# Kernel optimization log

Measured on AMD Instinct MI355X. Metric: run time of the kernel, lower is better.

Reference implementation:

```python
import jax, jax.numpy as jnp
import numpy as np

N_NODES = 50000
N_EDGES = 800000
IN_FEAT = 256
OUT_FEAT = 256
NUM_RELS = 64
NUM_BASES = 8


def setup_inputs() -> dict:
    key = jax.random.key(0)
    ks = jax.random.split(key, 9)
    x = jax.random.normal(ks[0], (N_NODES, IN_FEAT), dtype=jnp.float32)
    src = jax.random.randint(ks[1], (N_EDGES,), 0, N_NODES, dtype=jnp.int32)
    dst = jax.random.randint(ks[2], (N_EDGES,), 0, N_NODES, dtype=jnp.int32)
    etypes = jax.random.randint(ks[3], (N_EDGES,), 0, NUM_RELS, dtype=jnp.int32)
    norm = jax.random.uniform(ks[4], (N_EDGES, 1), dtype=jnp.float32)
    # glorot-style params
    s_w = (6.0 / (IN_FEAT + OUT_FEAT)) ** 0.5
    weight = jax.random.uniform(ks[5], (NUM_BASES, IN_FEAT, OUT_FEAT), jnp.float32, -s_w, s_w)
    s_c = (6.0 / (NUM_RELS + NUM_BASES)) ** 0.5
    w_comp = jax.random.uniform(ks[6], (NUM_RELS, NUM_BASES), jnp.float32, -s_c, s_c)
    h_bias = jnp.zeros((OUT_FEAT,), jnp.float32)
    loop_weight = jax.random.uniform(ks[7], (IN_FEAT, OUT_FEAT), jnp.float32, -s_w, s_w)
    return {"x": x, "src": src, "dst": dst, "etypes": etypes, "norm": norm,
            "weight": weight, "w_comp": w_comp, "h_bias": h_bias,
            "loop_weight": loop_weight}


def reference(x, src, dst, etypes, norm, weight, w_comp, h_bias, loop_weight):
    # Basis regularizer with num_bases < num_rels:
    #   W_r = sum_b w_comp[r, b] * V_b
    # Per-edge message: msg_e = (x[src_e] @ W_{etype_e}) * norm_e,
    # aggregated by sum onto destination nodes. Since the map is linear,
    # we aggregate per basis first, then apply V_b (8 dense GEMMs).
    n_nodes = x.shape[0]
    coef = w_comp[etypes]                      # [E, B] per-edge basis coeffs
    xs = x[src] * norm                         # [E, D] normalized source feats
    out = jnp.zeros((n_nodes, weight.shape[2]), x.dtype)
    for b in range(weight.shape[0]):           # small fixed loop over bases
        agg = jax.ops.segment_sum(xs * coef[:, b:b + 1], dst,
                                  num_segments=n_nodes)   # [N, D]
        out = out + agg @ weight[b]            # [N, O]
    out = out + h_bias + x @ loop_weight       # bias + self-loop
    return jax.nn.relu(out)
```

## Files before the change

kernel.cpp:

```cpp
#include <hip/hip_runtime.h>
#include <hip/hip_bf16.h>
#include <stdint.h>

#define N_NODES 50000
#define N_EDGES 800000
#define IN_FEAT 256
#define OUT_FEAT 256
#define NUM_RELS 64
#define NUM_BASES 8
#define KTOT 2304
#define KAGG 2048
#define MP 50048
#define SCAN_BLKS 196

typedef __attribute__((ext_vector_type(8))) __bf16 bf16x8;
typedef __attribute__((ext_vector_type(4))) __bf16 bf16x4;
typedef __attribute__((ext_vector_type(4))) float f32x4;
typedef __attribute__((ext_vector_type(2))) float f32x2;

static __device__ __forceinline__ void gload_lds16(const void* g, void* l) {
  auto gp = (const __attribute__((address_space(1))) void*)(uintptr_t)g;
  auto lp = (__attribute__((address_space(3))) void*)(uint32_t)(uintptr_t)l;
  __builtin_amdgcn_global_load_lds(gp, lp, 16, 0, 0);
}

__global__ void k_prex(const float* __restrict__ x, __bf16* __restrict__ xb) {
  int i = blockIdx.x * 256 + threadIdx.x;
  const float4* xp = (const float4*)x;
  float4 u = xp[i * 2], v = xp[i * 2 + 1];
  bf16x8 o;
  o[0] = (__bf16)u.x; o[1] = (__bf16)u.y; o[2] = (__bf16)u.z; o[3] = (__bf16)u.w;
  o[4] = (__bf16)v.x; o[5] = (__bf16)v.y; o[6] = (__bf16)v.z; o[7] = (__bf16)v.w;
  *(bf16x8*)(xb + (size_t)i * 8) = o;
}

__global__ void k_count(const int* __restrict__ dst, int* __restrict__ deg) {
  int e = blockIdx.x * 256 + threadIdx.x;
  atomicAdd(&deg[dst[e]], 1);
}

__global__ void k_scan1(const int* __restrict__ deg, int* __restrict__ offs,
                        int* __restrict__ bsum) {
  __shared__ int s[256];
  int t = threadIdx.x;
  int i = blockIdx.x * 256 + t;
  int v = (i < N_NODES) ? deg[i] : 0;
  s[t] = v;
  __syncthreads();
  for (int d = 1; d < 256; d <<= 1) {
    int y = (t >= d) ? s[t - d] : 0;
    __syncthreads();
    s[t] += y;
    __syncthreads();
  }
  if (i < N_NODES) offs[i] = s[t] - v;
  if (t == 255) bsum[blockIdx.x] = s[255];
}

__global__ void k_scan3(int* __restrict__ offs, const int* __restrict__ bsum,
                        int* __restrict__ fill) {
  __shared__ int s[256];
  int t = threadIdx.x;
  s[t] = (t < SCAN_BLKS && t < blockIdx.x) ? bsum[t] : 0;
  __syncthreads();
  for (int d = 128; d; d >>= 1) {
    if (t < d) s[t] += s[t + d];
    __syncthreads();
  }
  int base = s[0];
  int i = blockIdx.x * 256 + t;
  if (i < N_NODES) {
    int o = offs[i] + base;
    offs[i] = o;
    fill[i] = o;
  }
}

__global__ void k_scatter(const int* __restrict__ dst, const int* __restrict__ srcv,
                          const int* __restrict__ ety, const float* __restrict__ norm,
                          int* __restrict__ fill, uint2* __restrict__ erec) {
  int e = blockIdx.x * 256 + threadIdx.x;
  int pos = atomicAdd(&fill[dst[e]], 1);
  erec[pos] = make_uint2((unsigned)srcv[e] | ((unsigned)ety[e] << 16),
                         __float_as_uint(norm[e]));
}

#define AGG_BODY(RX, RY, XV)                                                  \
  do {                                                                        \
    int et_ = (RX) >> 16;                                                     \
    float nm_ = __uint_as_float(RY);                                          \
    f32x2 v0_ = {__uint_as_float((XV).x << 16) * nm_,                         \
                 __uint_as_float((XV).x & 0xffff0000u) * nm_};                 \
    f32x2 v1_ = {__uint_as_float((XV).y << 16) * nm_,                         \
                 __uint_as_float((XV).y & 0xffff0000u) * nm_};                 \
    f32x4 cl_ = *(const f32x4*)&wc[et_ * 8];                                  \
    f32x4 ch_ = *(const f32x4*)&wc[et_ * 8 + 4];                              \
    _Pragma("unroll") for (int b = 0; b < 4; ++b) {                           \
      acc[b][0] += v0_ * cl_[b];                                              \
      acc[b][1] += v1_ * cl_[b];                                              \
      acc[b + 4][0] += v0_ * ch_[b];                                          \
      acc[b + 4][1] += v1_ * ch_[b];                                          \
    }                                                                         \
  } while (0)

__global__ __launch_bounds__(256) void k_agg(
    const __bf16* __restrict__ xb, const float* __restrict__ w_comp,
    const int* __restrict__ offs, const int* __restrict__ fin,
    const uint2* __restrict__ erec, __bf16* __restrict__ A) {
  __shared__ float wc[NUM_RELS * NUM_BASES];
  int t = threadIdx.x;
  wc[t] = w_comp[t];
  wc[t + 256] = w_comp[t + 256];
  __syncthreads();

  int wid = t >> 6, lane = t & 63;
  int node = blockIdx.x * 4 + wid;

  f32x2 acc[NUM_BASES][2];
#pragma unroll
  for (int b = 0; b < NUM_BASES; ++b) {
    acc[b][0] = f32x2{0.f, 0.f};
    acc[b][1] = f32x2{0.f, 0.f};
  }

  int i0 = offs[node];
  int cnt = fin[node] - i0;
  const uint2* rp = erec + i0;
  int lo4 = lane * 4;

  int i = 0;
  for (; i + 8 <= cnt; i += 8) {
    uint2 r[8];
#pragma unroll
    for (int j = 0; j < 8; ++j) r[j] = rp[i + j];
    uint2 xv[8];
#pragma unroll
    for (int j = 0; j < 8; ++j)
      xv[j] = *(const uint2*)(xb + (size_t)(r[j].x & 0xffff) * IN_FEAT + lo4);
#pragma unroll
    for (int j = 0; j < 8; ++j) AGG_BODY(r[j].x, r[j].y, xv[j]);
  }
  for (; i + 4 <= cnt; i += 4) {
    uint2 r[4];
#pragma unroll
    for (int j = 0; j < 4; ++j) r[j] = rp[i + j];
    uint2 xv[4];
#pragma unroll
    for (int j = 0; j < 4; ++j)
      xv[j] = *(const uint2*)(xb + (size_t)(r[j].x & 0xffff) * IN_FEAT + lo4);
#pragma unroll
    for (int j = 0; j < 4; ++j) AGG_BODY(r[j].x, r[j].y, xv[j]);
  }
  for (; i < cnt; ++i) {
    uint2 r = rp[i];
    uint2 xv = *(const uint2*)(xb + (size_t)(r.x & 0xffff) * IN_FEAT + lo4);
    AGG_BODY(r.x, r.y, xv);
  }

  __bf16* Ar = A + (size_t)node * KAGG + lo4;
#pragma unroll
  for (int b = 0; b < NUM_BASES; ++b) {
    bf16x4 o;
    o[0] = (__bf16)acc[b][0][0];
    o[1] = (__bf16)acc[b][0][1];
    o[2] = (__bf16)acc[b][1][0];
    o[3] = (__bf16)acc[b][1][1];
    *(bf16x4*)(Ar + b * 256) = o;
  }
}

__global__ void k_prepw(const float* __restrict__ weight, const float* __restrict__ loop_w,
                        __bf16* __restrict__ Wt) {
  int o = blockIdx.x;
  int t = threadIdx.x;
#pragma unroll
  for (int c = 0; c < 9; ++c) {
    int r = c * 256 + t;
    float v = (r < 2048) ? weight[(size_t)r * 256 + o]
                         : loop_w[(size_t)(r - 2048) * 256 + o];
    Wt[(size_t)o * KTOT + r] = (__bf16)v;
  }
}

__global__ __launch_bounds__(256, 1) void k_gemm(const __bf16* __restrict__ A,
                                                 const __bf16* __restrict__ xb,
                                                 const __bf16* __restrict__ Wt,
                                                 const float* __restrict__ bias,
                                                 float* __restrict__ out) {
  __shared__ __align__(16) __bf16 sA[3 * 128 * 64];
  __shared__ __align__(16) __bf16 sB[3 * 256 * 64];

  int t = threadIdx.x;
  int wid = t >> 6, lane = t & 63;
  int tm = blockIdx.x;
  int wr = wid >> 1, wc = wid & 1;
  int rfw = __builtin_amdgcn_readfirstlane(wid);

  f32x4 acc[4][8];
#pragma unroll
  for (int m = 0; m < 4; ++m)
#pragma unroll
    for (int n = 0; n < 8; ++n) acc[m][n] = f32x4{0.f, 0.f, 0.f, 0.f};

  int frow = lane & 15;
  int g = lane >> 4;
  int f7 = lane & 7;
  int kb0 = ((g ^ f7) << 4);
  int kb1 = (((4 + g) ^ f7) << 4);

  int qoff = ((t & 7) ^ ((t >> 3) & 7)) * 8;
  const __bf16* gaP[4];
  const __bf16* gxP[4];
#pragma unroll
  for (int it = 0; it < 4; ++it) {
    int row = it * 32 + (t >> 3);
    gaP[it] = A + (size_t)(tm * 128 + row) * KAGG + qoff;
    gxP[it] = xb + (size_t)(tm * 128 + row) * IN_FEAT + qoff;
  }
  const __bf16* gbP[8];
#pragma unroll
  for (int it = 0; it < 8; ++it) {
    int row = it * 32 + (t >> 3);
    gbP[it] = Wt + (size_t)row * KTOT + qoff;
  }

#define VMWAIT(N) asm volatile("s_waitcnt vmcnt(" #N ")" ::: "memory")
#define BARRIER()                                   \
  do {                                              \
    asm volatile("" ::: "memory");                  \
    __builtin_amdgcn_s_barrier();                   \
    asm volatile("" ::: "memory");                  \
  } while (0)

#define STAGE(KT, BUF)                                                        \
  do {                                                                        \
    int k0_ = (KT) * 64;                                                      \
    char* bA_ = (char*)sA + (BUF) * 16384;                                    \
    char* bB_ = (char*)sB + (BUF) * 32768;                                    \
    if ((KT) < 32) {                                                          \
      _Pragma("unroll") for (int it = 0; it < 4; ++it)                        \
          gload_lds16(gaP[it] + k0_, bA_ + (it * 256 + rfw * 64) * 16);       \
    } else {                                                                  \
      int kx_ = k0_ - KAGG;                                                   \
      _Pragma("unroll") for (int it = 0; it < 4; ++it)                        \
          gload_lds16(gxP[it] + kx_, bA_ + (it * 256 + rfw * 64) * 16);       \
    }                                                                         \
    _Pragma("unroll") for (int it = 0; it < 8; ++it)                          \
        gload_lds16(gbP[it] + k0_, bB_ + (it * 256 + rfw * 64) * 16);         \
  } while (0)

#define COMPUTE(BUF)                                                          \
  do {                                                                        \
    const char* bA_ = (const char*)sA + (BUF) * 16384;                        \
    const char* bB_ = (const char*)sB + (BUF) * 32768;                        \
    {                                                                         \
      bf16x8 af[4], bfr[8];                                                   \
      _Pragma("unroll") for (int m = 0; m < 4; ++m)                           \
          af[m] = *(const bf16x8*)(bA_ + (wr * 64 + m * 16 + frow) * 128 + kb0);\
      _Pragma("unroll") for (int n = 0; n < 8; ++n)                           \
          bfr[n] = *(const bf16x8*)(bB_ + (wc * 128 + n * 16 + frow) * 128 + kb0);\
      _Pragma("unroll") for (int m = 0; m < 4; ++m)                           \
          _Pragma("unroll") for (int n = 0; n < 8; ++n)                       \
              acc[m][n] = __builtin_amdgcn_mfma_f32_16x16x32_bf16(            \
                  af[m], bfr[n], acc[m][n], 0, 0, 0);                         \
    }                                                                         \
    {                                                                         \
      bf16x8 af[4], bfr[8];                                                   \
      _Pragma("unroll") for (int m = 0; m < 4; ++m)                           \
          af[m] = *(const bf16x8*)(bA_ + (wr * 64 + m * 16 + frow) * 128 + kb1);\
      _Pragma("unroll") for (int n = 0; n < 8; ++n)                           \
          bfr[n] = *(const bf16x8*)(bB_ + (wc * 128 + n * 16 + frow) * 128 + kb1);\
      _Pragma("unroll") for (int m = 0; m < 4; ++m)                           \
          _Pragma("unroll") for (int n = 0; n < 8; ++n)                       \
              acc[m][n] = __builtin_amdgcn_mfma_f32_16x16x32_bf16(            \
                  af[m], bfr[n], acc[m][n], 0, 0, 0);                         \
    }                                                                         \
  } while (0)

  STAGE(0, 0);
  STAGE(1, 1);
  STAGE(2, 2);

#define STEP(KT, BUF)                                                         \
  do {                                                                        \
    VMWAIT(24);          \
    BARRIER();                       \
    COMPUTE(BUF);                                                             \
    BARRIER();               \
    STAGE((KT) + 3, BUF);                                                     \
  } while (0)

  for (int k3 = 0; k3 < 33; k3 += 3) {
    STEP(k3 + 0, 0);
    STEP(k3 + 1, 1);
    STEP(k3 + 2, 2);
  }
  VMWAIT(24); BARRIER(); COMPUTE(0);
  VMWAIT(12); BARRIER(); COMPUTE(1);
  VMWAIT(0);  BARRIER(); COMPUTE(2);
#undef STEP
#undef STAGE
#undef COMPUTE
#undef VMWAIT
#undef BARRIER

  int r0 = (lane >> 4) * 4;
  int c0 = lane & 15;
#pragma unroll
  for (int m = 0; m < 4; ++m) {
    int rowb = tm * 128 + wr * 64 + m * 16 + r0;
#pragma unroll
    for (int n = 0; n < 8; ++n) {
      int col = wc * 128 + n * 16 + c0;
      float bv = bias[col];
#pragma unroll
      for (int r = 0; r < 4; ++r) {
        int row = rowb + r;
        if (row < N_NODES) {
          float v = acc[m][n][r] + bv;
          out[(size_t)row * OUT_FEAT + col] = v > 0.f ? v : 0.f;
        }
      }
    }
  }
}

extern "C" void kernel_launch(void* const* d_in, const int* in_sizes, int n_in,
                              void* d_out, int out_size, void* d_ws, size_t ws_size,
                              hipStream_t stream) {
  const float* x      = (const float*)d_in[0];
  const int*   src    = (const int*)d_in[1];
  const int*   dst    = (const int*)d_in[2];
  const int*   ety    = (const int*)d_in[3];
  const float* norm   = (const float*)d_in[4];
  const float* weight = (const float*)d_in[5];
  const float* w_comp = (const float*)d_in[6];
  const float* h_bias = (const float*)d_in[7];
  const float* loop_w = (const float*)d_in[8];
  float* out = (float*)d_out;

  char* ws = (char*)d_ws;
  __bf16* A  = (__bf16*)ws;
  size_t off = (size_t)MP * KAGG * 2;
  __bf16* xb = (__bf16*)(ws + off);
  off += (size_t)MP * IN_FEAT * 2;
  __bf16* Wt = (__bf16*)(ws + off);
  off += (size_t)256 * KTOT * 2;
  uint2* erec = (uint2*)(ws + off);
  off += (size_t)N_EDGES * 8;
  int* deg   = (int*)(ws + off);
  int* offs  = deg + N_NODES;
  int* fill  = offs + N_NODES;
  int* bsum  = fill + N_NODES;

  hipMemsetAsync(deg, 0, N_NODES * sizeof(int), stream);
  k_prex<<<(N_NODES * IN_FEAT / 8) / 256, 256, 0, stream>>>(x, xb);
  k_count<<<N_EDGES / 256, 256, 0, stream>>>(dst, deg);
  k_scan1<<<SCAN_BLKS, 256, 0, stream>>>(deg, offs, bsum);
  k_scan3<<<SCAN_BLKS, 256, 0, stream>>>(offs, bsum, fill);
  k_scatter<<<N_EDGES / 256, 256, 0, stream>>>(dst, src, ety, norm, fill, erec);
  k_agg<<<N_NODES / 4, 256, 0, stream>>>(xb, w_comp, offs, fill, erec, A);
  k_prepw<<<256, 256, 0, stream>>>(weight, loop_w, Wt);
  k_gemm<<<MP / 128, 256, 0, stream>>>(A, xb, Wt, h_bias, out);
}
```

Baseline: 328.7 us.

## Use 256x256 GEMM tile with 8 waves and interleaved double-buffered schedule

The fused GEMM is reworked to process 256-row tiles with 512 threads, a 2-buffer LDS pipeline, and an interleaved schedule that splits each k-step into four MFMA groups. Global-to-LDS loads for the next tiles are issued between them, and MFMA sections run at raised wave priority. This is meant to improve overlap of loads with matrix math and raise reuse of the weight tile. In exchange it halves the number of blocks, which can leave CUs idle, and the padded row count grows.

```diff
diff --git a/kernel.cpp b/kernel.cpp
--- a/kernel.cpp
+++ b/kernel.cpp
@@ -10,7 +10,8 @@
 #define NUM_BASES 8
 #define KTOT 2304
 #define KAGG 2048
-#define MP 50048
+#define MP 50176
+#define NT 36
 #define SCAN_BLKS 196
 
 typedef __attribute__((ext_vector_type(8))) __bf16 bf16x8;
@@ -182,136 +183,159 @@
   }
 }
 
-__global__ __launch_bounds__(256, 1) void k_gemm(const __bf16* __restrict__ A,
+__global__ __launch_bounds__(512, 1) void k_gemm(const __bf16* __restrict__ A,
                                                  const __bf16* __restrict__ xb,
                                                  const __bf16* __restrict__ Wt,
                                                  const float* __restrict__ bias,
                                                  float* __restrict__ out) {
-  __shared__ __align__(16) __bf16 sA[3 * 128 * 64];
-  __shared__ __align__(16) __bf16 sB[3 * 256 * 64];
+  __shared__ __align__(16) __bf16 sA[2 * 256 * 64];
+  __shared__ __align__(16) __bf16 sB[2 * 256 * 64];
 
   int t = threadIdx.x;
   int wid = t >> 6, lane = t & 63;
   int tm = blockIdx.x;
-  int wr = wid >> 1, wc = wid & 1;
+  int wr = wid >> 2;
+  int wcol = wid & 3;
   int rfw = __builtin_amdgcn_readfirstlane(wid);
 
-  f32x4 acc[4][8];
-#pragma unroll
-  for (int m = 0; m < 4; ++m)
-#pragma unroll
-    for (int n = 0; n < 8; ++n) acc[m][n] = f32x4{0.f, 0.f, 0.f, 0.f};
+  f32x4 acc[8][4];
+#pragma unroll
+  for (int m = 0; m < 8; ++m)
+#pragma unroll
+    for (int n = 0; n < 4; ++n) acc[m][n] = f32x4{0.f, 0.f, 0.f, 0.f};
 
   int frow = lane & 15;
   int g = lane >> 4;
-  int f7 = lane & 7;
+  int f7 = frow & 7;
   int kb0 = ((g ^ f7) << 4);
   int kb1 = (((4 + g) ^ f7) << 4);
 
-  int qoff = ((t & 7) ^ ((t >> 3) & 7)) * 8;
-  const __bf16* gaP[4];
-  const __bf16* gxP[4];
-#pragma unroll
-  for (int it = 0; it < 4; ++it) {
-    int row = it * 32 + (t >> 3);
-    gaP[it] = A + (size_t)(tm * 128 + row) * KAGG + qoff;
-    gxP[it] = xb + (size_t)(tm * 128 + row) * IN_FEAT + qoff;
-  }
-  const __bf16* gbP[8];
-#pragma unroll
-  for (int it = 0; it < 8; ++it) {
-    int row = it * 32 + (t >> 3);
-    gbP[it] = Wt + (size_t)row * KTOT + qoff;
-  }
+  int rh = t >> 3;
+  int qoff = ((t & 7) ^ (rh & 7)) * 8;
+  const __bf16* gA[2][2];
+  const __bf16* gX[2][2];
+  const __bf16* gB[2][2];
+#pragma unroll
+  for (int h = 0; h < 2; ++h)
+#pragma unroll
+    for (int it = 0; it < 2; ++it) {
+      int row = h * 128 + it * 64 + rh;
+      gA[h][it] = A + (size_t)(tm * 256 + row) * KAGG + qoff;
+      gX[h][it] = xb + (size_t)(tm * 256 + row) * IN_FEAT + qoff;
+      gB[h][it] = Wt + (size_t)row * KTOT + qoff;
+    }
+
+  bf16x8 af[4][2];
+  bf16x8 bh0[2][2], bh1[2][2];
 
 #define VMWAIT(N) asm volatile("s_waitcnt vmcnt(" #N ")" ::: "memory")
-#define BARRIER()                                   \
+#define BAR()                                       \
   do {                                              \
     asm volatile("" ::: "memory");                  \
     __builtin_amdgcn_s_barrier();                   \
     asm volatile("" ::: "memory");                  \
   } while (0)
-
-#define STAGE(KT, BUF)                                                        \
-  do {                                                                        \
-    int k0_ = (KT) * 64;                                                      \
-    char* bA_ = (char*)sA + (BUF) * 16384;                                    \
-    char* bB_ = (char*)sB + (BUF) * 32768;                                    \
-    if ((KT) < 32) {                                                          \
-      _Pragma("unroll") for (int it = 0; it < 4; ++it)                        \
-          gload_lds16(gaP[it] + k0_, bA_ + (it * 256 + rfw * 64) * 16);       \
+#define PRIO(N) __builtin_amdgcn_s_setprio(N)
+
+#define STAGE_A(H, U, BUF)                                                    \
+  do {                                                                        \
+    char* d_ = (char*)sA + (BUF) * 32768 + (H) * 16384 + rfw * 1024;          \
+    if ((U) < 32) {                                                           \
+      int ko_ = (U) * 64;                                                     \
+      gload_lds16(gA[H][0] + ko_, d_);                                        \
+      gload_lds16(gA[H][1] + ko_, d_ + 8192);                                 \
     } else {                                                                  \
-      int kx_ = k0_ - KAGG;                                                   \
-      _Pragma("unroll") for (int it = 0; it < 4; ++it)                        \
-          gload_lds16(gxP[it] + kx_, bA_ + (it * 256 + rfw * 64) * 16);       \
-    }                                                                         \
-    _Pragma("unroll") for (int it = 0; it < 8; ++it)                          \
-        gload_lds16(gbP[it] + k0_, bB_ + (it * 256 + rfw * 64) * 16);         \
-  } while (0)
-
-#define COMPUTE(BUF)                                                          \
-  do {                                                                        \
-    const char* bA_ = (const char*)sA + (BUF) * 16384;                        \
-    const char* bB_ = (const char*)sB + (BUF) * 32768;                        \
-    {                                                                         \
-      bf16x8 af[4], bfr[8];                                                   \
-      _Pragma("unroll") for (int m = 0; m < 4; ++m)                           \
-          af[m] = *(const bf16x8*)(bA_ + (wr * 64 + m * 16 + frow) * 128 + kb0);\
-      _Pragma("unroll") for (int n = 0; n < 8; ++n)                           \
-          bfr[n] = *(const bf16x8*)(bB_ + (wc * 128 + n * 16 + frow) * 128 + kb0);\
-      _Pragma("unroll") for (int m = 0; m < 4; ++m)                           \
-          _Pragma("unroll") for (int n = 0; n < 8; ++n)                       \
-              acc[m][n] = __builtin_amdgcn_mfma_f32_16x16x32_bf16(            \
-                  af[m], bfr[n], acc[m][n], 0, 0, 0);                         \
-    }                                                                         \
-    {                                                                         \
-      bf16x8 af[4], bfr[8];                                                   \
-      _Pragma("unroll") for (int m = 0; m < 4; ++m)                           \
-          af[m] = *(const bf16x8*)(bA_ + (wr * 64 + m * 16 + frow) * 128 + kb1);\
-      _Pragma("unroll") for (int n = 0; n < 8; ++n)                           \
-          bfr[n] = *(const bf16x8*)(bB_ + (wc * 128 + n * 16 + frow) * 128 + kb1);\
-      _Pragma("unroll") for (int m = 0; m < 4; ++m)                           \
-          _Pragma("unroll") for (int n = 0; n < 8; ++n)                       \
-              acc[m][n] = __builtin_amdgcn_mfma_f32_16x16x32_bf16(            \
-                  af[m], bfr[n], acc[m][n], 0, 0, 0);                         \
-    }                                                                         \
-  } while (0)
-
-  STAGE(0, 0);
-  STAGE(1, 1);
-  STAGE(2, 2);
-
-#define STEP(KT, BUF)                                                         \
-  do {                                                                        \
-    VMWAIT(24);          \
-    BARRIER();                       \
-    COMPUTE(BUF);                                                             \
-    BARRIER();               \
-    STAGE((KT) + 3, BUF);                                                     \
-  } while (0)
-
-  for (int k3 = 0; k3 < 33; k3 += 3) {
-    STEP(k3 + 0, 0);
-    STEP(k3 + 1, 1);
-    STEP(k3 + 2, 2);
-  }
-  VMWAIT(24); BARRIER(); COMPUTE(0);
-  VMWAIT(12); BARRIER(); COMPUTE(1);
-  VMWAIT(0);  BARRIER(); COMPUTE(2);
-#undef STEP
-#undef STAGE
-#undef COMPUTE
+      int ko_ = ((U) - 32) * 64;                                              \
+      gload_lds16(gX[H][0] + ko_, d_);                                        \
+      gload_lds16(gX[H][1] + ko_, d_ + 8192);                                 \
+    }                                                                         \
+  } while (0)
+
+#define STAGE_B(H, U, BUF)                                                    \
+  do {                                                                        \
+    char* d_ = (char*)sB + (BUF) * 32768 + (H) * 16384 + rfw * 1024;          \
+    int ko_ = (U) * 64;                                                       \
+    gload_lds16(gB[H][0] + ko_, d_);                                          \
+    gload_lds16(gB[H][1] + ko_, d_ + 8192);                                   \
+  } while (0)
+
+#define READ_A(BUF, MS)                                                       \
+  do {                                                                        \
+    const char* b_ = (const char*)sA + (BUF) * 32768;                         \
+    _Pragma("unroll") for (int mf = 0; mf < 4; ++mf) {                        \
+      int r_ = wr * 128 + (MS) * 64 + mf * 16 + frow;                         \
+      af[mf][0] = *(const bf16x8*)(b_ + r_ * 128 + kb0);                      \
+      af[mf][1] = *(const bf16x8*)(b_ + r_ * 128 + kb1);                      \
+    }                                                                         \
+  } while (0)
+
+#define READ_B(BUF, NH, DST)                                                  \
+  do {                                                                        \
+    const char* b_ = (const char*)sB + (BUF) * 32768;                         \
+    _Pragma("unroll") for (int nf = 0; nf < 2; ++nf) {                        \
+      int r_ = wcol * 64 + ((NH) * 2 + nf) * 16 + frow;                       \
+      DST[nf][0] = *(const bf16x8*)(b_ + r_ * 128 + kb0);                     \
+      DST[nf][1] = *(const bf16x8*)(b_ + r_ * 128 + kb1);                     \
+    }                                                                         \
+  } while (0)
+
+#define MFMA16(MS, NH, BS)                                                    \
+  do {                                                                        \
+    _Pragma("unroll") for (int mf = 0; mf < 4; ++mf)                          \
+    _Pragma("unroll") for (int nf = 0; nf < 2; ++nf) {                        \
+      acc[(MS) * 4 + mf][(NH) * 2 + nf] =                                     \
+          __builtin_amdgcn_mfma_f32_16x16x32_bf16(                            \
+              af[mf][0], BS[nf][0], acc[(MS) * 4 + mf][(NH) * 2 + nf], 0, 0, 0);\
+      acc[(MS) * 4 + mf][(NH) * 2 + nf] =                                     \
+          __builtin_amdgcn_mfma_f32_16x16x32_bf16(                            \
+              af[mf][1], BS[nf][1], acc[(MS) * 4 + mf][(NH) * 2 + nf], 0, 0, 0);\
+    }                                                                         \
+  } while (0)
+
+  STAGE_A(0, 0, 0);
+  STAGE_A(1, 0, 0);
+  STAGE_B(0, 0, 0);
+  STAGE_B(1, 0, 0);
+  STAGE_A(0, 1, 1);
+  VMWAIT(2);
+  BAR();
+
+  for (int kt = 0; kt < NT; ++kt) {
+    int cb = kt & 1, nb = cb ^ 1;
+    int u1 = (kt + 1 < NT) ? kt + 1 : NT - 1;
+    int u2 = (kt + 2 < NT) ? kt + 2 : NT - 1;
+    READ_A(cb, 0);
+    READ_B(cb, 0, bh0);
+    STAGE_A(1, u1, nb);
+    BAR(); PRIO(1); MFMA16(0, 0, bh0); PRIO(0); BAR();
+    READ_B(cb, 1, bh1);
+    STAGE_B(0, u1, nb);
+    BAR(); PRIO(1); MFMA16(0, 1, bh1); PRIO(0); BAR();
+    READ_A(cb, 1);
+    STAGE_B(1, u1, nb);
+    BAR(); PRIO(1); MFMA16(1, 0, bh0); PRIO(0); BAR();
+    STAGE_A(0, u2, cb);
+    BAR(); PRIO(1); MFMA16(1, 1, bh1); PRIO(0);
+    VMWAIT(2);
+    BAR();
+  }
+#undef STAGE_A
+#undef STAGE_B
+#undef READ_A
+#undef READ_B
+#undef MFMA16
 #undef VMWAIT
-#undef BARRIER
+#undef BAR
+#undef PRIO
 
   int r0 = (lane >> 4) * 4;
   int c0 = lane & 15;
 #pragma unroll
-  for (int m = 0; m < 4; ++m) {
-    int rowb = tm * 128 + wr * 64 + m * 16 + r0;
-#pragma unroll
-    for (int n = 0; n < 8; ++n) {
-      int col = wc * 128 + n * 16 + c0;
+  for (int m = 0; m < 8; ++m) {
+    int rowb = tm * 256 + wr * 128 + m * 16 + r0;
+#pragma unroll
+    for (int n = 0; n < 4; ++n) {
+      int col = wcol * 64 + n * 16 + c0;
       float bv = bias[col];
 #pragma unroll
       for (int r = 0; r < 4; ++r) {
@@ -361,5 +385,5 @@
   k_scatter<<<N_EDGES / 256, 256, 0, stream>>>(dst, src, ety, norm, fill, erec);
   k_agg<<<N_NODES / 4, 256, 0, stream>>>(xb, w_comp, offs, fill, erec, A);
   k_prepw<<<256, 256, 0, stream>>>(weight, loop_w, Wt);
-  k_gemm<<<MP / 128, 256, 0, stream>>>(A, xb, Wt, h_bias, out);
-}
+  k_gemm<<<MP / 256, 512, 0, stream>>>(A, xb, Wt, h_bias, out);
+}
```

Measured after the change: 294.3 us. 1.12x faster.
